# Performance work log

Hardware: AMD Instinct MI355X
Metric: run time of the kernel (lower is better)

## Reference

```python
import jax, jax.numpy as jnp
import numpy as np

H = 256
LATENT = 128
NODE_FEATS = (12, 5, 4)
EDGE_FEATS = (5, 4)
END_NODE = NODE_FEATS[0] - 1
MAX_NODES = 64


def setup_inputs() -> dict:
    key = jax.random.key(0)
    ks = iter(jax.random.split(key, 40))
    def rn(shape, s=0.1):
        return jax.random.normal(next(ks), shape, dtype=jnp.float32) * s
    inp = {
        "z": jax.random.normal(next(ks), (1, LATENT), dtype=jnp.float32),
        "lp_w": rn((H, LATENT)), "lp_b": rn((H,)),
        "nWih": rn((3 * H, H)), "nWhh": rn((3 * H, H)), "nbih": rn((3 * H,)), "nbhh": rn((3 * H,)),
        "eWih": rn((3 * H, H)), "eWhh": rn((3 * H, H)), "ebih": rn((3 * H,)), "ebhh": rn((3 * H,)),
    }
    for j, f in enumerate(NODE_FEATS):
        inp[f"nc{j}_w"] = rn((f, H)); inp[f"nc{j}_b"] = rn((f,))
    for j, f in enumerate(EDGE_FEATS):
        inp[f"ec{j}_w"] = rn((f, H)); inp[f"ec{j}_b"] = rn((f,))
    inp["max_nodes"] = MAX_NODES
    return inp


def _gru(x, h, Wih, Whh, bih, bhh):
    # torch.nn.GRU single step, single layer. x,h: (1,H)
    gi = x @ Wih.T + bih
    gh = h @ Whh.T + bhh
    ir, iz, inn = jnp.split(gi, 3, axis=-1)
    hr, hz, hn = jnp.split(gh, 3, axis=-1)
    r = jax.nn.sigmoid(ir + hr)
    zg = jax.nn.sigmoid(iz + hz)
    n = jnp.tanh(inn + r * hn)
    return (1.0 - zg) * n + zg * h


def _classify(emb, W, b):
    # Linear -> softmax -> (max prob, argmax), batch=1 -> scalars
    p = jax.nn.softmax(emb @ W.T + b, axis=-1)[0]
    return jnp.max(p), jnp.argmax(p)


def _generate(z, lp_w, lp_b, nWih, nWhh, nbih, nbhh, eWih, eWhh, ebih, ebhh,
              nc0_w, nc0_b, nc1_w, nc1_b, nc2_w, nc2_b,
              ec0_w, ec0_b, ec1_w, ec1_b, max_nodes):
    node_cls = ((nc0_w, nc0_b), (nc1_w, nc1_b), (nc2_w, nc2_b))
    edge_cls = ((ec0_w, ec0_b), (ec1_w, ec1_b))
    h0 = z @ lp_w.T + lp_b                     # latent_project; set_context
    buf0 = jnp.zeros((max_nodes, 1, H), z.dtype)  # node embedding history

    def step(carry, i):
        h, buf, done = carry
        x = jnp.where(i == 0, jnp.zeros((1, H), z.dtype), buf[jnp.maximum(i - 1, 0)])
        h1 = _gru(x, h, nWih, nWhh, nbih, nbhh)   # node_celli.forward_unit; emb = h1
        nps, nis = zip(*[_classify(h1, W, b) for W, b in node_cls])
        nprobs = jnp.stack(nps)                   # (3,)
        nidxs = jnp.stack(nis)                    # (3,) int
        is_end = nidxs[0] == END_NODE

        # edge cell: seq over previous node embeddings, most recent first
        def estep(he, t):
            valid = t < i
            src = jnp.clip(i - 1 - t, 0, max_nodes - 1)
            he2 = _gru(buf[src], he, eWih, eWhh, ebih, ebhh)
            he_new = jnp.where(valid, he2, he)
            eps, eis = zip(*[_classify(he_new, W, b) for W, b in edge_cls])
            return he_new, (jnp.stack(eps), jnp.stack(eis))

        he_fin, (ep_t, ei_t) = jax.lax.scan(estep, h1, jnp.arange(max_nodes))
        # reindex: edge for source node j was produced at inner step t = i-1-j
        js = jnp.arange(max_nodes)
        ts = jnp.clip(i - 1 - js, 0, max_nodes - 1)
        ep_row = ep_t[ts]                          # (max_nodes, 2)
        ei_row = ei_t[ts]
        vj = js < i
        no_edges = jnp.all(jnp.where(vj, ei_row[:, 0] == 0, True)) & (i > 0)

        active = jnp.logical_not(done)
        node_ok = active & jnp.logical_not(is_end) & jnp.logical_not(no_edges)
        done_new = done | is_end | no_edges

        h_next = jnp.where(node_ok & (i > 0), he_fin, h1)  # node hidden <- edge hidden
        h_next = jnp.where(active, h_next, h)
        buf_new = buf.at[i].set(jnp.where(node_ok, h1, buf[i]))

        edge_valid = vj & node_ok & (i > 0)
        out = (jnp.where(node_ok, nprobs, 0.0), nidxs, node_ok,
               jnp.where(edge_valid[:, None], ep_row, 0.0), ei_row, edge_valid)
        return (h_next, buf_new, done_new), out

    _, outs = jax.lax.scan(step, (h0, buf0, jnp.zeros((), bool)), jnp.arange(max_nodes))
    # node_probs (M,3), node_idxs (M,3), node_valid (M,),
    # edge_probs (M,M,2), edge_idxs (M,M,2), edge_valid (M,M)
    return outs


def reference(z, lp_w, lp_b, nWih, nWhh, nbih, nbhh, eWih, eWhh, ebih, ebhh,
              nc0_w, nc0_b, nc1_w, nc1_b, nc2_w, nc2_b,
              ec0_w, ec0_b, ec1_w, ec1_b, max_nodes):
    return _generate(z, lp_w, lp_b, nWih, nWhh, nbih, nbhh, eWih, eWhh, ebih, ebhh,
                     nc0_w, nc0_b, nc1_w, nc1_b, nc2_w, nc2_b,
                     ec0_w, ec0_b, ec1_w, ec1_b, max_nodes)
```

## Files before the change

### kernel.cpp

```cpp
#include <hip/hip_runtime.h>
#include <stdint.h>
#include <cstddef>


typedef unsigned int u32;

#define H 256
#define HL 128
#define G3 768
#define NW 16
#define SL 16
#define MAXN 64
#define NSTATE (1 + MAXN + (MAXN*(MAXN-1))/2)
#define SENTU 0xFFFFFFFFu
#define DEADV 0x0000DEADu
#define PAD 264

#define WG_CLS NW
#define WG_HELP0 (NW+1)
#define NHELP_PER 6
#define NROLE (WG_HELP0 + 2*NHELP_PER)
#define NWG 256

#define NP_OFF 0
#define NI_OFF 192
#define NV_OFF 384
#define EP_OFF 448
#define EI_OFF (EP_OFF + MAXN*MAXN*2)
#define EV_OFF (EI_OFF + MAXN*MAXN*2)

struct Wksp {
  float hP[NSTATE][H];
  float hS[NSTATE][H];
  float gi_e[MAXN][G3];
  float gi_n[MAXN][G3];
  u32 decP[MAXN];
  u32 decS[MAXN];
  u32 winner;
  u32 padw[7];
  u32 ticket[8];
};

union Shm {
  struct {
    float whe[3*SL*PAD];
    float whn[3*SL*PAD];
    float hcur[2][H];
    float bihe[3*SL], bhhe[3*SL], bihn[3*SL], bhhn[3*SL];
    float zv[HL];
    u32 dec;
  } w;
  struct {
    float cw[30*H];
    float cb[30];
    float hc[H];
    float logits[30];
    float resp[5];
    int   resi[5];
    float ept[MAXN][2];
    int   eit[MAXN][2];
  } c;
  struct { float h1[H]; } hp;
};

__device__ __forceinline__ u32 ld_sc0(const u32* p) {
  u32 v;
  asm volatile("global_load_dword %0, %1, off sc0\n\ts_waitcnt vmcnt(0)"
               : "=&v"(v) : "v"(p) : "memory");
  return v;
}
__device__ __forceinline__ void st_sc0(u32* p, u32 v) {
  asm volatile("global_store_dword %0, %1, off sc0" :: "v"(p), "v"(v) : "memory");
}
__device__ __forceinline__ u32 ld_ag(const u32* p) {
  return __hip_atomic_load(p, __ATOMIC_RELAXED, __HIP_MEMORY_SCOPE_AGENT);
}
__device__ __forceinline__ void st_ag(u32* p, u32 v) {
  __hip_atomic_store(p, v, __ATOMIC_RELAXED, __HIP_MEMORY_SCOPE_AGENT);
}
__device__ __forceinline__ void pub2(u32* pp, u32* sp, u32 v, bool sc) {
  if (sc) st_sc0(pp, v);
  st_ag(sp, v);
}
__device__ __forceinline__ void pub2f(float* pp, float* sp, float x, bool sc) {
  pub2((u32*)pp, (u32*)sp, __float_as_uint(x), sc);
}
__device__ __forceinline__ u32 spin2(const u32* pp, const u32* sp, bool sc) {
  if (sc) {
    #pragma unroll 1
    for (int i = 0; i < 16; ++i) {
      const u32 v = ld_sc0(pp);
      if (v != SENTU) return v;
    }
  }
  u32 v = ld_ag(sp);
  while (v == SENTU) v = ld_ag(sp);
  return v;
}
__device__ __forceinline__ float spin2f(const float* pp, const float* sp, bool sc) {
  return __uint_as_float(spin2((const u32*)pp, (const u32*)sp, sc));
}
__device__ __forceinline__ float spinf(const float* p) {
  u32 v = ld_ag((const u32*)p);
  while (v == SENTU) v = ld_ag((const u32*)p);
  return __uint_as_float(v);
}
__device__ __forceinline__ void pubf(float* p, float x) { st_ag((u32*)p, __float_as_uint(x)); }
__device__ __forceinline__ float sigm(float x) { return 1.0f / (1.0f + expf(-x)); }

__global__ __launch_bounds__(256)
void Generator_34746285425383_kernel(
    const float* __restrict__ z, const float* __restrict__ lp_w, const float* __restrict__ lp_b,
    const float* __restrict__ nWih, const float* __restrict__ nWhh,
    const float* __restrict__ nbih, const float* __restrict__ nbhh,
    const float* __restrict__ eWih, const float* __restrict__ eWhh,
    const float* __restrict__ ebih, const float* __restrict__ ebhh,
    const float* __restrict__ nc0w, const float* __restrict__ nc0b,
    const float* __restrict__ nc1w, const float* __restrict__ nc1b,
    const float* __restrict__ nc2w, const float* __restrict__ nc2b,
    const float* __restrict__ ec0w, const float* __restrict__ ec0b,
    const float* __restrict__ ec1w, const float* __restrict__ ec1b,
    float* __restrict__ out, Wksp* __restrict__ ws)
{
  __shared__ Shm S;
  __shared__ int role_s, mode_s;
  const int tid = threadIdx.x;

  if (tid == 0) {
    u32 xcc;
    asm volatile("s_getreg_b32 %0, hwreg(HW_REG_XCC_ID)" : "=s"(xcc));
    xcc &= 7u;
    const u32 slot = __hip_atomic_fetch_add(&ws->ticket[xcc], 1u,
                        __ATOMIC_RELAXED, __HIP_MEMORY_SCOPE_AGENT);
    if (slot == NROLE - 1) {
      u32 exp = SENTU;
      __hip_atomic_compare_exchange_strong(&ws->winner, &exp, xcc,
          __ATOMIC_RELAXED, __ATOMIC_RELAXED, __HIP_MEMORY_SCOPE_AGENT);
    }
    u32 wv = ld_ag(&ws->winner);
    int iters = 0;
    while (wv == SENTU) {
      ++iters;
      if (iters > 1500 && blockIdx.x == 0) {
        u32 exp = SENTU;
        __hip_atomic_compare_exchange_strong(&ws->winner, &exp, DEADV,
            __ATOMIC_RELAXED, __ATOMIC_RELAXED, __HIP_MEMORY_SCOPE_AGENT);
      }
      wv = ld_ag(&ws->winner);
    }
    if (wv <= 7u) { role_s = (wv == xcc && slot < NROLE) ? (int)slot : -1; mode_s = 1; }
    else          { role_s = ((int)blockIdx.x < NROLE) ? (int)blockIdx.x : -1; mode_s = 0; }
  }
  __syncthreads();
  const int bid = role_s;
  const bool sc = (mode_s != 0);
  if (bid < 0) return;

  if (bid < NW) {
    const int w = bid, g = tid >> 4, c = tid & 15;
    const int k = w * SL + g;
    for (int r = 0; r < 3 * SL; ++r) {
      const int gate = r / SL, gg = r % SL;
      const int grow = gate * H + (w * SL + gg);
      for (int col = tid; col < H; col += 256) {
        S.w.whe[r * PAD + col] = eWhh[grow * H + col];
        S.w.whn[r * PAD + col] = nWhh[grow * H + col];
      }
    }
    if (tid < 3 * SL) {
      const int gate = tid / SL, gg = tid % SL;
      const int grow = gate * H + w * SL + gg;
      S.w.bihe[tid] = ebih[grow]; S.w.bhhe[tid] = ebhh[grow];
      S.w.bihn[tid] = nbih[grow]; S.w.bhhn[tid] = nbhh[grow];
    }
    if (tid < HL) S.w.zv[tid] = z[tid];
    __syncthreads();

    {
      float p = 0.f;
      for (int it = 0; it < 8; ++it) {
        const int col = c + 16 * it;
        p += S.w.zv[col] * lp_w[k * HL + col];
      }
      for (int off = 1; off < 16; off <<= 1) p += __shfl_xor(p, off);
      if (c == 0) pub2f(&ws->hP[0][k], &ws->hS[0][k], p + lp_b[k], sc);
    }

    int m = 1, idx_carry = 0;
    bool done = false;
    unsigned long long valid = 0ull;
    float pg0 = 0.f, pg1 = 0.f, pg2 = 0.f;
    const float* pga = nullptr;

    for (int i = 0; i < MAXN; ++i) {
      for (int t = -1; t < i; ++t) {
        const bool is_node = (t < 0);
        const int hidx = is_node ? idx_carry : (m - 1);
        const int src  = is_node ? (i - 1) : (i - 1 - t);
        float* hc = S.w.hcur[m & 1];
        hc[tid] = spin2f(&ws->hP[hidx][tid], &ws->hS[hidx][tid], sc);
        float gi0 = 0.f, gi1 = 0.f, gi2 = 0.f;
        const bool use_gi = (src >= 0) && ((valid >> src) & 1ull);
        if (use_gi) {
          gi0 = pg0; gi1 = pg1; gi2 = pg2;
          if (__float_as_uint(gi0) == SENTU) gi0 = spinf(&pga[0 * H + k]);
          if (__float_as_uint(gi1) == SENTU) gi1 = spinf(&pga[1 * H + k]);
          if (__float_as_uint(gi2) == SENTU) gi2 = spinf(&pga[2 * H + k]);
        }
        __syncthreads();
        const float* Wl = is_node ? S.w.whn : S.w.whe;
        float p0 = 0.f, p1 = 0.f, p2 = 0.f;
        #pragma unroll
        for (int it = 0; it < 16; ++it) {
          const int col = c + 16 * it;
          const float hv = hc[col];
          p0 += Wl[(0 * SL + g) * PAD + col] * hv;
          p1 += Wl[(1 * SL + g) * PAD + col] * hv;
          p2 += Wl[(2 * SL + g) * PAD + col] * hv;
        }
        for (int off = 1; off < 16; off <<= 1) {
          p0 += __shfl_xor(p0, off);
          p1 += __shfl_xor(p1, off);
          p2 += __shfl_xor(p2, off);
        }
        const float* bih = is_node ? S.w.bihn : S.w.bihe;
        const float* bhh = is_node ? S.w.bhhn : S.w.bhhe;
        const float rr = sigm(gi0 + bih[0 * SL + g] + p0 + bhh[0 * SL + g]);
        const float zz = sigm(gi1 + bih[1 * SL + g] + p1 + bhh[1 * SL + g]);
        const float nn = tanhf(gi2 + bih[2 * SL + g] + rr * (p2 + bhh[2 * SL + g]));
        const float hp = (1.f - zz) * nn + zz * hc[k];
        if (c == 0) pub2f(&ws->hP[m][k], &ws->hS[m][k], hp, sc);
        {
          int ni = i, nt = t + 1;
          if (nt >= i) { ni = i + 1; nt = -1; }
          if (ni < MAXN) {
            const bool nnode = (nt < 0);
            const int nsrc = nnode ? (ni - 1) : (ni - 1 - nt);
            if (nsrc >= 0) {
              pga = nnode ? ws->gi_n[nsrc] : ws->gi_e[nsrc];
              pg0 = __builtin_nontemporal_load(&pga[0 * H + k]);
              pg1 = __builtin_nontemporal_load(&pga[1 * H + k]);
              pg2 = __builtin_nontemporal_load(&pga[2 * H + k]);
            }
          }
        }
        ++m;
      }
      if (tid == 0) S.w.dec = spin2(&ws->decP[i], &ws->decS[i], sc);
      __syncthreads();
      const u32 dec = S.w.dec;
      const bool is_end   = (dec >> 1) & 1u;
      const bool no_edges = (dec >> 2) & 1u;
      const bool active   = !done;
      const bool node_ok  = active && !is_end && !no_edges;
      if (node_ok) valid |= (1ull << i);
      const int s_end = m - 1, node_m = m - 1 - i;
      if (active) idx_carry = (node_ok && i > 0) ? s_end : node_m;
      done = done || is_end || no_edges;
    }

  } else if (bid == WG_CLS) {
    const int g = tid >> 4, c = tid & 15;
    const float* wsrc[5] = { nc0w, nc1w, nc2w, ec0w, ec1w };
    const float* bsrc[5] = { nc0b, nc1b, nc2b, ec0b, ec1b };
    const int hbase[5] = { 0, 12, 17, 21, 26 };
    const int hlen[5]  = { 12, 5, 4, 5, 4 };
    for (int hh = 0; hh < 5; ++hh)
      for (int r = 0; r < hlen[hh]; ++r)
        for (int col = tid; col < H; col += 256)
          S.c.cw[(hbase[hh] + r) * H + col] = wsrc[hh][r * H + col];
    if (tid < 30) {
      const int hh = tid < 12 ? 0 : tid < 17 ? 1 : tid < 21 ? 2 : tid < 26 ? 3 : 4;
      S.c.cb[tid] = bsrc[hh][tid - hbase[hh]];
    }
    __syncthreads();

    int m = 1;
    bool done = false;
    for (int i = 0; i < MAXN; ++i) {
      float npmax[3]; int nidx[3];
      bool is_end = false, andacc = true;
      for (int t = -1; t < i; ++t) {
        S.c.hc[tid] = spin2f(&ws->hP[m][tid], &ws->hS[m][tid], sc);
        __syncthreads();
        for (int rsel = 0; rsel < 2; ++rsel) {
          const int r = g + 16 * rsel;
          float p = 0.f;
          if (r < 30) {
            #pragma unroll
            for (int it = 0; it < 16; ++it) {
              const int col = c + 16 * it;
              p += S.c.cw[r * H + col] * S.c.hc[col];
            }
          }
          for (int off = 1; off < 16; off <<= 1) p += __shfl_xor(p, off);
          if (r < 30 && c == 0) S.c.logits[r] = p + S.c.cb[r];
        }
        __syncthreads();
        if (tid < 5) {
          const int base = hbase[tid], len = hlen[tid];
          float best = S.c.logits[base]; int bi = 0;
          for (int j = 1; j < len; ++j) {
            const float l = S.c.logits[base + j];
            if (l > best) { best = l; bi = j; }
          }
          float s = 0.f;
          for (int j = 0; j < len; ++j) s += expf(S.c.logits[base + j] - best);
          S.c.resp[tid] = 1.0f / s;
          S.c.resi[tid] = bi;
        }
        __syncthreads();
        if (t < 0) {
          npmax[0] = S.c.resp[0]; npmax[1] = S.c.resp[1]; npmax[2] = S.c.resp[2];
          nidx[0] = S.c.resi[0]; nidx[1] = S.c.resi[1]; nidx[2] = S.c.resi[2];
          is_end = (S.c.resi[0] == 11);
          if (i == 0 && tid == 0) {
            S.c.ept[0][0] = S.c.resp[3]; S.c.ept[0][1] = S.c.resp[4];
            S.c.eit[0][0] = S.c.resi[3]; S.c.eit[0][1] = S.c.resi[4];
          }
        } else {
          if (tid == 0) {
            S.c.ept[t][0] = S.c.resp[3]; S.c.ept[t][1] = S.c.resp[4];
            S.c.eit[t][0] = S.c.resi[3]; S.c.eit[t][1] = S.c.resi[4];
          }
          andacc = andacc && (S.c.resi[3] == 0);
        }
        __syncthreads();
        ++m;
      }
      const bool no_edges = (i > 0) && andacc;
      const bool active = !done;
      const bool node_ok = active && !is_end && !no_edges;
      if (tid == 0) {
        const u32 d = 1u | (is_end ? 2u : 0u) | (no_edges ? 4u : 0u);
        pub2(&ws->decP[i], &ws->decS[i], d, sc);
      }
      if (tid < MAXN) {
        const int j = tid;
        const bool vj = j < i;
        const bool ev = vj && node_ok && (i > 0);
        const int tt = vj ? (i - 1 - j) : 0;
        out[EP_OFF + (i * MAXN + j) * 2 + 0] = ev ? S.c.ept[tt][0] : 0.f;
        out[EP_OFF + (i * MAXN + j) * 2 + 1] = ev ? S.c.ept[tt][1] : 0.f;
        out[EI_OFF + (i * MAXN + j) * 2 + 0] = (float)S.c.eit[tt][0];
        out[EI_OFF + (i * MAXN + j) * 2 + 1] = (float)S.c.eit[tt][1];
        out[EV_OFF + i * MAXN + j] = ev ? 1.f : 0.f;
      } else if (tid < MAXN + 8) {
        const int q = tid - MAXN;
        if (q < 3)       out[NP_OFF + i * 3 + q]       = node_ok ? npmax[q] : 0.f;
        else if (q < 6)  out[NI_OFF + i * 3 + (q - 3)] = (float)nidx[q - 3];
        else if (q == 6) out[NV_OFF + i]               = node_ok ? 1.f : 0.f;
      }
      done = done || is_end || no_edges;
      __syncthreads();
    }

  } else {
    const int e = bid - WG_HELP0;
    const bool is_edge = (e < NHELP_PER);
    const int rowbase = (e % NHELP_PER) * 128;
    const float* Wih = is_edge ? eWih : nWih;
    float* gdst = is_edge ? &ws->gi_e[0][0] : &ws->gi_n[0][0];
    const int g = tid >> 4, c = tid & 15;
    int m_node = 1;
    for (int i = 0; i < MAXN; ++i) {
      S.hp.h1[tid] = spinf(&ws->hS[m_node][tid]);
      __syncthreads();
      for (int rr = 0; rr < 8; ++rr) {
        const int row = rowbase + g * 8 + rr;
        float p = 0.f;
        #pragma unroll
        for (int u = 0; u < 4; ++u) {
          const float4 wv = *(const float4*)&Wih[row * H + c * 16 + u * 4];
          p += wv.x * S.hp.h1[c * 16 + u * 4 + 0]
             + wv.y * S.hp.h1[c * 16 + u * 4 + 1]
             + wv.z * S.hp.h1[c * 16 + u * 4 + 2]
             + wv.w * S.hp.h1[c * 16 + u * 4 + 3];
        }
        for (int off = 1; off < 16; off <<= 1) p += __shfl_xor(p, off);
        if (c == 0) pubf(&gdst[i * G3 + row], p);
      }
      __syncthreads();
      m_node += 1 + i;
    }
  }
}

extern "C" void kernel_launch(void* const* d_in, const int* in_sizes, int n_in,
                              void* d_out, int out_size, void* d_ws, size_t ws_size,
                              hipStream_t stream) {
  hipMemsetAsync(d_ws, 0xFF, offsetof(Wksp, ticket), stream);
  hipMemsetAsync((char*)d_ws + offsetof(Wksp, ticket), 0,
                 sizeof(Wksp) - offsetof(Wksp, ticket), stream);
  Generator_34746285425383_kernel<<<dim3(NWG), dim3(256), 0, stream>>>(
      (const float*)d_in[0],  (const float*)d_in[1],  (const float*)d_in[2],
      (const float*)d_in[3],  (const float*)d_in[4],  (const float*)d_in[5],
      (const float*)d_in[6],  (const float*)d_in[7],  (const float*)d_in[8],
      (const float*)d_in[9],  (const float*)d_in[10],
      (const float*)d_in[11], (const float*)d_in[12],
      (const float*)d_in[13], (const float*)d_in[14],
      (const float*)d_in[15], (const float*)d_in[16],
      (const float*)d_in[17], (const float*)d_in[18],
      (const float*)d_in[19], (const float*)d_in[20],
      (float*)d_out, (Wksp*)d_ws);
}
```

Baseline: 5.275 ms.

## Parallelize classifier softmax with wave shuffles and cut per-step barriers

The classifier workgroup now computes the five argmax/softmax heads across 64 lanes using shuffle reductions instead of five serial threads. It double-buffers the hidden-state copy so two of the three barriers per step can be removed. The no-edges test becomes one ballot per node instead of a per-step accumulator. Publishing is split across lanes 0 and 1, only two lanes per row read the precomputed gate inputs, and helper spin loops add s_sleep to reduce polling pressure. The risks are more reliance on the double buffer being race-free and added wake-up latency for the helper workgroups.

```diff
diff --git a/kernel.cpp b/kernel.cpp
--- a/kernel.cpp
+++ b/kernel.cpp
@@ -53,12 +53,12 @@
   struct {
     float cw[30*H];
     float cb[30];
-    float hc[H];
-    float logits[30];
-    float resp[5];
-    int   resi[5];
+    float hc[2][H];
+    float logits[32];
+    float np[3]; int ni[3];
     float ept[MAXN][2];
     int   eit[MAXN][2];
+    u32 isend, bflag;
   } c;
   struct { float h1[H]; } hp;
 };
@@ -81,9 +81,6 @@
 __device__ __forceinline__ void pub2(u32* pp, u32* sp, u32 v, bool sc) {
   if (sc) st_sc0(pp, v);
   st_ag(sp, v);
-}
-__device__ __forceinline__ void pub2f(float* pp, float* sp, float x, bool sc) {
-  pub2((u32*)pp, (u32*)sp, __float_as_uint(x), sc);
 }
 __device__ __forceinline__ u32 spin2(const u32* pp, const u32* sp, bool sc) {
   if (sc) {
@@ -103,6 +100,14 @@
 __device__ __forceinline__ float spinf(const float* p) {
   u32 v = ld_ag((const u32*)p);
   while (v == SENTU) v = ld_ag((const u32*)p);
+  return __uint_as_float(v);
+}
+__device__ __forceinline__ float spinf_slow(const float* p) {
+  u32 v = ld_ag((const u32*)p);
+  while (v == SENTU) {
+    __builtin_amdgcn_s_sleep(1);
+    v = ld_ag((const u32*)p);
+  }
   return __uint_as_float(v);
 }
 __device__ __forceinline__ void pubf(float* p, float x) { st_ag((u32*)p, __float_as_uint(x)); }
@@ -159,6 +164,7 @@
   if (bid < NW) {
     const int w = bid, g = tid >> 4, c = tid & 15;
     const int k = w * SL + g;
+    const bool gl = (c < 2);
     for (int r = 0; r < 3 * SL; ++r) {
       const int gate = r / SL, gg = r % SL;
       const int grow = gate * H + (w * SL + gg);
@@ -183,7 +189,9 @@
         p += S.w.zv[col] * lp_w[k * HL + col];
       }
       for (int off = 1; off < 16; off <<= 1) p += __shfl_xor(p, off);
-      if (c == 0) pub2f(&ws->hP[0][k], &ws->hS[0][k], p + lp_b[k], sc);
+      const float h0 = p + lp_b[k];
+      if (c == 0 && sc) st_sc0((u32*)&ws->hP[0][k], __float_as_uint(h0));
+      if (c == 1)       st_ag((u32*)&ws->hS[0][k], __float_as_uint(h0));
     }
 
     int m = 1, idx_carry = 0;
@@ -201,7 +209,7 @@
         hc[tid] = spin2f(&ws->hP[hidx][tid], &ws->hS[hidx][tid], sc);
         float gi0 = 0.f, gi1 = 0.f, gi2 = 0.f;
         const bool use_gi = (src >= 0) && ((valid >> src) & 1ull);
-        if (use_gi) {
+        if (gl && use_gi) {
           gi0 = pg0; gi1 = pg1; gi2 = pg2;
           if (__float_as_uint(gi0) == SENTU) gi0 = spinf(&pga[0 * H + k]);
           if (__float_as_uint(gi1) == SENTU) gi1 = spinf(&pga[1 * H + k]);
@@ -229,8 +237,9 @@
         const float zz = sigm(gi1 + bih[1 * SL + g] + p1 + bhh[1 * SL + g]);
         const float nn = tanhf(gi2 + bih[2 * SL + g] + rr * (p2 + bhh[2 * SL + g]));
         const float hp = (1.f - zz) * nn + zz * hc[k];
-        if (c == 0) pub2f(&ws->hP[m][k], &ws->hS[m][k], hp, sc);
-        {
+        if (c == 0 && sc) st_sc0((u32*)&ws->hP[m][k], __float_as_uint(hp));
+        if (c == 1)       st_ag((u32*)&ws->hS[m][k], __float_as_uint(hp));
+        if (gl) {
           int ni = i, nt = t + 1;
           if (nt >= i) { ni = i + 1; nt = -1; }
           if (ni < MAXN) {
@@ -278,10 +287,9 @@
     int m = 1;
     bool done = false;
     for (int i = 0; i < MAXN; ++i) {
-      float npmax[3]; int nidx[3];
-      bool is_end = false, andacc = true;
       for (int t = -1; t < i; ++t) {
-        S.c.hc[tid] = spin2f(&ws->hP[m][tid], &ws->hS[m][tid], sc);
+        float* hcb = S.c.hc[m & 1];
+        hcb[tid] = spin2f(&ws->hP[m][tid], &ws->hS[m][tid], sc);
         __syncthreads();
         for (int rsel = 0; rsel < 2; ++rsel) {
           const int r = g + 16 * rsel;
@@ -290,47 +298,67 @@
             #pragma unroll
             for (int it = 0; it < 16; ++it) {
               const int col = c + 16 * it;
-              p += S.c.cw[r * H + col] * S.c.hc[col];
+              p += S.c.cw[r * H + col] * hcb[col];
             }
           }
           for (int off = 1; off < 16; off <<= 1) p += __shfl_xor(p, off);
           if (r < 30 && c == 0) S.c.logits[r] = p + S.c.cb[r];
         }
         __syncthreads();
-        if (tid < 5) {
-          const int base = hbase[tid], len = hlen[tid];
-          float best = S.c.logits[base]; int bi = 0;
-          for (int j = 1; j < len; ++j) {
-            const float l = S.c.logits[base + j];
-            if (l > best) { best = l; bi = j; }
+        if (tid < 64) {
+          const int lane = tid;
+          int hh, j;
+          if (lane < 16)      { hh = 0; j = lane;      }
+          else if (lane < 24) { hh = 1; j = lane - 16; }
+          else if (lane < 32) { hh = 2; j = lane - 24; }
+          else if (lane < 40) { hh = 3; j = lane - 32; }
+          else if (lane < 48) { hh = 4; j = lane - 40; }
+          else                { hh = 4; j = 99; }
+          const int hb = hbase[hh], hl = hlen[hh];
+          const bool live = (j < hl);
+          const float myl = live ? S.c.logits[hb + j] : -3.4e38f;
+          float mx = myl; int idx = live ? j : 1000;
+          #pragma unroll
+          for (int mk = 1; mk <= 4; mk <<= 1) {
+            const float lv = __shfl_xor(mx, mk);
+            const int   iv = __shfl_xor(idx, mk);
+            if (lv > mx || (lv == mx && iv < idx)) { mx = lv; idx = iv; }
           }
-          float s = 0.f;
-          for (int j = 0; j < len; ++j) s += expf(S.c.logits[base + j] - best);
-          S.c.resp[tid] = 1.0f / s;
-          S.c.resi[tid] = bi;
-        }
-        __syncthreads();
-        if (t < 0) {
-          npmax[0] = S.c.resp[0]; npmax[1] = S.c.resp[1]; npmax[2] = S.c.resp[2];
-          nidx[0] = S.c.resi[0]; nidx[1] = S.c.resi[1]; nidx[2] = S.c.resi[2];
-          is_end = (S.c.resi[0] == 11);
-          if (i == 0 && tid == 0) {
-            S.c.ept[0][0] = S.c.resp[3]; S.c.ept[0][1] = S.c.resp[4];
-            S.c.eit[0][0] = S.c.resi[3]; S.c.eit[0][1] = S.c.resi[4];
+          { const float lv = __shfl_xor(mx, 8);
+            const int   iv = __shfl_xor(idx, 8);
+            if (lane < 16 && (lv > mx || (lv == mx && iv < idx))) { mx = lv; idx = iv; } }
+          float e = live ? expf(myl - mx) : 0.f;
+          #pragma unroll
+          for (int mk = 1; mk <= 4; mk <<= 1) e += __shfl_xor(e, mk);
+          { const float ev = __shfl_xor(e, 8); if (lane < 16) e += ev; }
+          const float pm = 1.0f / e;
+          if (t < 0) {
+            if (lane == 0)  { S.c.np[0] = pm; S.c.ni[0] = idx;
+                              S.c.isend = (idx == 11) ? 1u : 0u; }
+            if (lane == 16) { S.c.np[1] = pm; S.c.ni[1] = idx; }
+            if (lane == 24) { S.c.np[2] = pm; S.c.ni[2] = idx; }
+            if (i == 0) {
+              if (lane == 32) { S.c.ept[0][0] = pm; S.c.eit[0][0] = idx; }
+              if (lane == 40) { S.c.ept[0][1] = pm; S.c.eit[0][1] = idx; }
+            }
+          } else {
+            if (lane == 32) { S.c.ept[t][0] = pm; S.c.eit[t][0] = idx; }
+            if (lane == 40) { S.c.ept[t][1] = pm; S.c.eit[t][1] = idx; }
           }
-        } else {
-          if (tid == 0) {
-            S.c.ept[t][0] = S.c.resp[3]; S.c.ept[t][1] = S.c.resp[4];
-            S.c.eit[t][0] = S.c.resi[3]; S.c.eit[t][1] = S.c.resi[4];
-          }
-          andacc = andacc && (S.c.resi[3] == 0);
-        }
-        __syncthreads();
+        }
         ++m;
       }
-      const bool no_edges = (i > 0) && andacc;
-      const bool active = !done;
-      const bool node_ok = active && !is_end && !no_edges;
+      __syncthreads();
+      if (tid < 64) {
+        const bool myok = (tid < i) ? (S.c.eit[tid][0] == 0) : true;
+        const unsigned long long b = __ballot(myok);
+        if (tid == 0) S.c.bflag = ((b == ~0ull) && (i > 0)) ? 1u : 0u;
+      }
+      __syncthreads();
+      const bool is_end   = (S.c.isend != 0u);
+      const bool no_edges = (S.c.bflag != 0u);
+      const bool active   = !done;
+      const bool node_ok  = active && !is_end && !no_edges;
       if (tid == 0) {
         const u32 d = 1u | (is_end ? 2u : 0u) | (no_edges ? 4u : 0u);
         pub2(&ws->decP[i], &ws->decS[i], d, sc);
@@ -347,8 +375,8 @@
         out[EV_OFF + i * MAXN + j] = ev ? 1.f : 0.f;
       } else if (tid < MAXN + 8) {
         const int q = tid - MAXN;
-        if (q < 3)       out[NP_OFF + i * 3 + q]       = node_ok ? npmax[q] : 0.f;
-        else if (q < 6)  out[NI_OFF + i * 3 + (q - 3)] = (float)nidx[q - 3];
+        if (q < 3)       out[NP_OFF + i * 3 + q]       = node_ok ? S.c.np[q] : 0.f;
+        else if (q < 6)  out[NI_OFF + i * 3 + (q - 3)] = (float)S.c.ni[q - 3];
         else if (q == 6) out[NV_OFF + i]               = node_ok ? 1.f : 0.f;
       }
       done = done || is_end || no_edges;
@@ -364,7 +392,7 @@
     const int g = tid >> 4, c = tid & 15;
     int m_node = 1;
     for (int i = 0; i < MAXN; ++i) {
-      S.hp.h1[tid] = spinf(&ws->hS[m_node][tid]);
+      S.hp.h1[tid] = spinf_slow(&ws->hS[m_node][tid]);
       __syncthreads();
       for (int rr = 0; rr < 8; ++rr) {
         const int row = rowbase + g * 8 + rr;
```

After: 5.048 ms. 4.3% less time.
